# Performance work log

Measured on AMD Instinct MI355X. Metric: run time of the kernel, lower is better.

Reference implementation:

```python
import jax, jax.numpy as jnp
import numpy as np

# Constants derived from init_kwargs (sample_rate=16000, frame_ms=20, hop_ms=None)
SR = 16000
FRAME = 320            # frame_length = int(sr*frame_ms/1000); also NCCF frame_size (frame_time = hop/sr)
HOP = 320
FREQ_LOW, FREQ_HIGH = 85, 3400          # torchaudio detect_pitch_frequency defaults
LAGS = int(np.ceil(SR / FREQ_LOW))      # 189 lags checked
LAG_MIN = int(np.ceil(SR / FREQ_HIGH))  # 5
WIN_MED = 30                            # win_length for median smoothing
EPS = 1e-9


def _nccf(audio):
    """Batched torchaudio _compute_nccf. audio: (B,T) -> (B,K,LAGS)."""
    B, T = audio.shape
    K = -(-T // FRAME)                       # num_of_frames = ceil(T/frame_size)
    p = LAGS + K * FRAME - T                 # right pad
    w = jnp.pad(audio, ((0, 0), (0, p)))
    # seg[b,k,j] = w[b, k*FRAME + j], j in [0, FRAME+LAGS)
    j = jnp.arange(K)[:, None] * FRAME + jnp.arange(FRAME + LAGS)[None, :]
    seg = w[:, j]                            # (B,K,FRAME+LAGS)
    s1 = seg[:, :, :FRAME]                   # (B,K,FRAME)   lag-independent frames
    li = jnp.arange(1, LAGS + 1)[:, None] + jnp.arange(FRAME)[None, :]   # (LAGS,FRAME)
    s2 = seg[:, :, li]                       # (B,K,LAGS,FRAME) shifted frames
    cross = jnp.einsum('bki,bkli->bkl', s1, s2)
    n1 = jnp.sqrt(jnp.einsum('bki,bki->bk', s1, s1))
    n2 = jnp.sqrt(jnp.einsum('bkli,bkli->bkl', s2, s2))
    # torchaudio: sum(s1*s2) / (eps+||s1||)^2 / (eps+||s2||)^2
    return cross / (EPS + n1[..., None]) ** 2 / (EPS + n2) ** 2


def _find_max_per_frame(nccf):
    """torchaudio _find_max_per_frame: prefer smaller near-max lag."""
    tail = nccf[..., LAG_MIN:]
    best_v, best_i = jnp.max(tail, -1), jnp.argmax(tail, -1)
    half_size = nccf.shape[-1] // 2
    half = nccf[..., LAG_MIN:half_size]
    half_v, half_i = jnp.max(half, -1), jnp.argmax(half, -1)
    mask = half_v > 0.99 * best_v
    idx = jnp.where(mask, half_i, best_i)
    return (idx + LAG_MIN + 1).astype(jnp.int32)   # +lag_min, +1 calibration offset


def _median_smoothing(idx):
    """torchaudio _median_smoothing: left replicate-pad, sliding lower-median."""
    pad = (WIN_MED - 1) // 2
    x = jnp.concatenate([jnp.repeat(idx[:, :1], pad, axis=1), idx], axis=1)  # (B,K+pad)
    nwin = x.shape[1] - WIN_MED + 1
    wi = jnp.arange(nwin)[:, None] + jnp.arange(WIN_MED)[None, :]
    win = x[:, wi]                                   # (B,nwin,WIN_MED)
    # torch.median returns the lower median for even window size
    return jnp.sort(win, -1)[..., (WIN_MED - 1) // 2]


def _forward(audio):
    nccf = _nccf(audio)
    idx = _median_smoothing(_find_max_per_frame(nccf))
    f0 = SR / (EPS + idx.astype(jnp.float32))        # (B, K-15)
    voiced = (f0 > 0).astype(jnp.float32)
    T = audio.shape[1]
    Ke = (T - FRAME) // HOP + 1
    fi = jnp.arange(Ke)[:, None] * HOP + jnp.arange(FRAME)[None, :]
    energy = jnp.mean(audio[:, fi] ** 2, axis=-1)    # (B, Ke)
    # train-mode whitening: masked mean/std (ddof=1) over voiced f0
    valid = (f0 > 0).astype(jnp.float32)
    n = jnp.sum(valid)
    mean = jnp.where(n > 0, jnp.sum(f0 * valid) / jnp.maximum(n, 1.0), 0.0)
    var = jnp.sum(((f0 - mean) ** 2) * valid) / jnp.maximum(n - 1.0, 1.0)
    std = jnp.where(n > 1, jnp.sqrt(var), 1.0)
    std = jnp.where(std == 0, 1.0, std)
    whiten = (f0 - mean) / std
    return f0, whiten, voiced, energy


def setup_inputs() -> dict:
    key = jax.random.key(0)
    audio = jax.random.normal(key, (8, 80000), dtype=jnp.float32)
    return {"audio": audio}


def reference(audio):
    # returns (f0_hz, f0_whiten, voiced_prob, energy)
    return _forward(audio)
```

## Files before the change

### kernel.cpp

```cpp
#include <hip/hip_runtime.h>
#include <math.h>

#define SRATE 16000
#define FRAME 320
#define LAGS 189
#define LAG_MIN 5
#define WIN_MED 30
#define BATCH 8
#define TLEN 80000
#define KFRAMES 250
#define NOUT 235
#define NTOT (BATCH * NOUT)
#define SEG (FRAME + LAGS)

__global__ __launch_bounds__(64) void nccf_best_kernel(
    const float* __restrict__ audio, int* __restrict__ best,
    float* __restrict__ out) {
  const int k = blockIdx.x;
  const int b = blockIdx.y;
  const float* row = audio + (size_t)b * TLEN;
  const int base = k * FRAME;

  __shared__ float sh[512];
  __shared__ float shv[LAGS];

  for (int c = threadIdx.x; c < 128; c += 64) {
    int j = 4 * c;
    float4 v;
    if (j + 3 < SEG && base + j + 3 < TLEN) {
      v = *(const float4*)(row + base + j);
    } else {
      v.x = (j + 0 < SEG && base + j + 0 < TLEN) ? row[base + j + 0] : 0.0f;
      v.y = (j + 1 < SEG && base + j + 1 < TLEN) ? row[base + j + 1] : 0.0f;
      v.z = (j + 2 < SEG && base + j + 2 < TLEN) ? row[base + j + 2] : 0.0f;
      v.w = (j + 3 < SEG && base + j + 3 < TLEN) ? row[base + j + 3] : 0.0f;
    }
    *(float4*)&sh[j] = v;
  }
  __syncthreads();

  const int t = threadIdx.x;
  if (t < 48) {
    float wv[8];
    *(float4*)&wv[0] = *(const float4*)&sh[4 * t];
    float cr[4] = {0.f, 0.f, 0.f, 0.f};
    float e2[4] = {0.f, 0.f, 0.f, 0.f};
    float e1 = 0.f;
    for (int i0 = 0; i0 < FRAME; i0 += 4) {
      float4 a = *(const float4*)&sh[i0];
      *(float4*)&wv[4] = *(const float4*)&sh[4 * t + i0 + 4];
      e1 += a.x * a.x + a.y * a.y + a.z * a.z + a.w * a.w;
      #pragma unroll
      for (int d = 0; d < 4; ++d) {
        float c0 = wv[d + 1], c1 = wv[d + 2], c2 = wv[d + 3], c3 = wv[d + 4];
        cr[d] += a.x * c0 + a.y * c1 + a.z * c2 + a.w * c3;
        e2[d] += c0 * c0 + c1 * c1 + c2 * c2 + c3 * c3;
      }
      wv[0] = wv[4]; wv[1] = wv[5]; wv[2] = wv[6]; wv[3] = wv[7];
    }
    float d1 = 1e-9f + sqrtf(e1);
    float inv1 = 1.0f / (d1 * d1);
    #pragma unroll
    for (int d = 0; d < 4; ++d) {
      int ll = 4 * t + d;
      if (ll < LAGS) {
        float d2 = 1e-9f + sqrtf(e2[d]);
        shv[ll] = cr[d] * inv1 / (d2 * d2);
      }
    }
    if (t == 0) out[3 * NTOT + b * KFRAMES + k] = e1 * (1.0f / FRAME);
  }
  __syncthreads();

  if (threadIdx.x == 0) {
    float best_v = -INFINITY; int best_l = LAG_MIN;
    float half_v = -INFINITY; int half_l = LAG_MIN;
    for (int ll = LAG_MIN; ll < LAGS; ++ll) {
      float v = shv[ll];
      if (v > best_v) { best_v = v; best_l = ll; }
      if (ll < (LAGS / 2) && v > half_v) { half_v = v; half_l = ll; }
    }
    int chosen = (half_v > 0.99f * best_v) ? half_l : best_l;
    best[b * KFRAMES + k] = chosen + 1;
  }
}

__global__ __launch_bounds__(256) void median_f0_kernel(
    const int* __restrict__ best, float* __restrict__ out) {
  const int w = blockIdx.x * 4 + (threadIdx.x >> 6);
  const int lane = threadIdx.x & 63;
  const int b = w / NOUT;
  const int t = w - b * NOUT;

  int v = 0x7fffffff;
  if (lane < WIN_MED) {
    int j = t + lane - 14;
    if (j < 0) j = 0;
    v = best[b * KFRAMES + j];
  }
  int c_lt = 0, c_le = 0;
  #pragma unroll
  for (int j = 0; j < WIN_MED; ++j) {
    int bv = __shfl(v, j, 64);
    c_lt += (bv < v) ? 1 : 0;
    c_le += (bv <= v) ? 1 : 0;
  }
  bool cond = (lane < WIN_MED) && (c_lt <= 14) && (c_le > 14);
  unsigned long long m = __ballot(cond);
  int sel = __ffsll((long long)m) - 1;
  int med = __shfl(v, sel, 64);
  if (lane == 0) {
    float f0 = 16000.0f / (1e-9f + (float)med);
    out[b * NOUT + t] = f0;
    out[2 * NTOT + b * NOUT + t] = 1.0f;
  }
}

__global__ __launch_bounds__(256) void whiten_kernel(float* __restrict__ out) {
  __shared__ double red[256];
  __shared__ double red2[256];
  const int t = threadIdx.x;
  double s = 0.0, s2 = 0.0;
  for (int i = t; i < NTOT; i += 256) {
    double f = (double)out[i];
    s += f; s2 += f * f;
  }
  red[t] = s; red2[t] = s2;
  __syncthreads();
  for (int st = 128; st > 0; st >>= 1) {
    if (t < st) { red[t] += red[t + st]; red2[t] += red2[t + st]; }
    __syncthreads();
  }
  __shared__ float fmean_s, finvsd_s;
  if (t == 0) {
    const double n = (double)NTOT;
    double mean = red[0] / n;
    double var = (red2[0] - n * mean * mean) / (n - 1.0);
    if (var < 0.0) var = 0.0;
    double sd = sqrt(var);
    fmean_s = (float)mean;
    finvsd_s = (sd == 0.0) ? 1.0f : (float)(1.0 / sd);
  }
  __syncthreads();
  float fmean = fmean_s, finvsd = finvsd_s;
  for (int i = t; i < NTOT; i += 256) {
    out[NTOT + i] = (out[i] - fmean) * finvsd;
  }
}

extern "C" void kernel_launch(void* const* d_in, const int* in_sizes, int n_in,
                              void* d_out, int out_size, void* d_ws, size_t ws_size,
                              hipStream_t stream) {
  const float* audio = (const float*)d_in[0];
  float* out = (float*)d_out;
  int* best = (int*)d_ws;

  dim3 g1(KFRAMES, BATCH);
  nccf_best_kernel<<<g1, 64, 0, stream>>>(audio, best, out);
  median_f0_kernel<<<(NTOT + 3) / 4, 256, 0, stream>>>(best, out);
  whiten_kernel<<<1, 256, 0, stream>>>(out);
}
```

Baseline: 86.64 us.

## Split NCCF frame sum across four wavefronts and parallelize argmax with shuffles

Each per-frame block now uses 256 threads. The four wavefronts each compute partial cross-correlation and energy sums over an 80-sample slice of the frame, and the partials are combined through shared memory. The serial single-thread lag scan is replaced by a wavefront-wide shuffle reduction that breaks ties toward the smaller index. This shortens the per-block serial critical path and raises occupancy, at the cost of extra shared memory, extra barriers, and a changed floating-point summation order.

```diff
diff --git a/kernel.cpp b/kernel.cpp
--- a/kernel.cpp
+++ b/kernel.cpp
@@ -13,7 +13,7 @@
 #define NTOT (BATCH * NOUT)
 #define SEG (FRAME + LAGS)
 
-__global__ __launch_bounds__(64) void nccf_best_kernel(
+__global__ __launch_bounds__(256) void nccf_best_kernel(
     const float* __restrict__ audio, int* __restrict__ best,
     float* __restrict__ out) {
   const int k = blockIdx.x;
@@ -22,10 +22,15 @@
   const int base = k * FRAME;
 
   __shared__ float sh[512];
-  __shared__ float shv[LAGS];
+  __shared__ float pcr[4][192];
+  __shared__ float pe2[4][192];
+  __shared__ float pe1[4];
+  __shared__ float shv[192];
 
-  for (int c = threadIdx.x; c < 128; c += 64) {
-    int j = 4 * c;
+  const int tid = threadIdx.x;
+
+  if (tid < 128) {
+    int j = 4 * tid;
     float4 v;
     if (j + 3 < SEG && base + j + 3 < TLEN) {
       v = *(const float4*)(row + base + j);
@@ -39,16 +44,19 @@
   }
   __syncthreads();
 
-  const int t = threadIdx.x;
-  if (t < 48) {
+  const int w = tid >> 6;
+  const int lane = tid & 63;
+
+  if (lane < 48) {
+    const int i0b = w * 80;
     float wv[8];
-    *(float4*)&wv[0] = *(const float4*)&sh[4 * t];
+    *(float4*)&wv[0] = *(const float4*)&sh[4 * lane + i0b];
     float cr[4] = {0.f, 0.f, 0.f, 0.f};
     float e2[4] = {0.f, 0.f, 0.f, 0.f};
     float e1 = 0.f;
-    for (int i0 = 0; i0 < FRAME; i0 += 4) {
-      float4 a = *(const float4*)&sh[i0];
-      *(float4*)&wv[4] = *(const float4*)&sh[4 * t + i0 + 4];
+    for (int ii = 0; ii < 80; ii += 4) {
+      float4 a = *(const float4*)&sh[i0b + ii];
+      *(float4*)&wv[4] = *(const float4*)&sh[4 * lane + i0b + ii + 4];
       e1 += a.x * a.x + a.y * a.y + a.z * a.z + a.w * a.w;
       #pragma unroll
       for (int d = 0; d < 4; ++d) {
@@ -58,30 +66,48 @@
       }
       wv[0] = wv[4]; wv[1] = wv[5]; wv[2] = wv[6]; wv[3] = wv[7];
     }
-    float d1 = 1e-9f + sqrtf(e1);
-    float inv1 = 1.0f / (d1 * d1);
-    #pragma unroll
-    for (int d = 0; d < 4; ++d) {
-      int ll = 4 * t + d;
-      if (ll < LAGS) {
-        float d2 = 1e-9f + sqrtf(e2[d]);
-        shv[ll] = cr[d] * inv1 / (d2 * d2);
-      }
-    }
-    if (t == 0) out[3 * NTOT + b * KFRAMES + k] = e1 * (1.0f / FRAME);
+    *(float4*)&pcr[w][4 * lane] = *(float4*)cr;
+    *(float4*)&pe2[w][4 * lane] = *(float4*)e2;
+    if (lane == 0) pe1[w] = e1;
   }
   __syncthreads();
 
-  if (threadIdx.x == 0) {
-    float best_v = -INFINITY; int best_l = LAG_MIN;
-    float half_v = -INFINITY; int half_l = LAG_MIN;
-    for (int ll = LAG_MIN; ll < LAGS; ++ll) {
-      float v = shv[ll];
-      if (v > best_v) { best_v = v; best_l = ll; }
-      if (ll < (LAGS / 2) && v > half_v) { half_v = v; half_l = ll; }
+  if (tid < LAGS) {
+    float crs = pcr[0][tid] + pcr[1][tid] + pcr[2][tid] + pcr[3][tid];
+    float e2s = pe2[0][tid] + pe2[1][tid] + pe2[2][tid] + pe2[3][tid];
+    float e1s = pe1[0] + pe1[1] + pe1[2] + pe1[3];
+    float d1 = 1e-9f + sqrtf(e1s);
+    float d2 = 1e-9f + sqrtf(e2s);
+    shv[tid] = crs / (d1 * d1) / (d2 * d2);
+    if (tid == 0) out[3 * NTOT + b * KFRAMES + k] = e1s * (1.0f / FRAME);
+  }
+  __syncthreads();
+
+  if (w == 0) {
+    float bv = -INFINITY; int bi = 0;
+    float hv = -INFINITY; int hi2 = 0;
+    #pragma unroll
+    for (int r = 0; r < 3; ++r) {
+      int ll = LAG_MIN + lane + 64 * r;
+      if (ll < LAGS) {
+        float v = shv[ll];
+        if (v > bv || (v == bv && ll < bi)) { bv = v; bi = ll; }
+        if (ll < (LAGS / 2) && (v > hv || (v == hv && ll < hi2))) { hv = v; hi2 = ll; }
+      }
     }
-    int chosen = (half_v > 0.99f * best_v) ? half_l : best_l;
-    best[b * KFRAMES + k] = chosen + 1;
+    #pragma unroll
+    for (int off = 32; off >= 1; off >>= 1) {
+      float ov = __shfl_xor(bv, off, 64);
+      int   oi = __shfl_xor(bi, off, 64);
+      if (ov > bv || (ov == bv && oi < bi)) { bv = ov; bi = oi; }
+      float ohv = __shfl_xor(hv, off, 64);
+      int   ohi = __shfl_xor(hi2, off, 64);
+      if (ohv > hv || (ohv == hv && ohi < hi2)) { hv = ohv; hi2 = ohi; }
+    }
+    if (lane == 0) {
+      int chosen = (hv > 0.99f * bv) ? hi2 : bi;
+      best[b * KFRAMES + k] = chosen + 1;
+    }
   }
 }
 
@@ -156,7 +182,7 @@
   int* best = (int*)d_ws;
 
   dim3 g1(KFRAMES, BATCH);
-  nccf_best_kernel<<<g1, 64, 0, stream>>>(audio, best, out);
+  nccf_best_kernel<<<g1, 256, 0, stream>>>(audio, best, out);
   median_f0_kernel<<<(NTOT + 3) / 4, 256, 0, stream>>>(best, out);
   whiten_kernel<<<1, 256, 0, stream>>>(out);
 }
```

Result: faster. 81.42 us (-6.0%).
